# Performance work log

Hardware: AMD Instinct MI355X
Metric: run time of the kernel (lower is better)

Reference implementation:

```python
import jax, jax.numpy as jnp
import numpy as np

LOSS_WEIGHT = 1.0
BIG = 1e9  # finite sentinel for masked-out pixels (avoids inf-grad NaNs)


def setup_inputs() -> dict:
    key = jax.random.key(0)
    k1, k2 = jax.random.split(key)
    B, N, H, W = 4, 6890, 64, 64
    vert2d = jax.random.uniform(k1, (B, N, 2), dtype=jnp.float32) * jnp.array([W, H], jnp.float32)
    mask = jax.random.randint(k2, (B, H, W), 0, 2, dtype=jnp.int32)
    return {"vert2d": vert2d, "mask": mask}


def reference(vert2d, mask):
    B, N, _ = vert2d.shape
    _, H, W = mask.shape
    scale = jnp.array([W, H], vert2d.dtype)
    v = vert2d / scale  # [B,N,2], normalized
    # all pixel coords as (x, y), normalized -- the dense equivalent of torch.where points
    ys, xs = jnp.meshgrid(jnp.arange(H), jnp.arange(W), indexing="ij")
    pts = (jnp.stack([xs.ravel(), ys.ravel()], axis=-1).astype(v.dtype) / scale)  # [HW,2]
    valid = (mask.reshape(B, -1) > 0)  # [B,HW] boolean membership of each pixel
    # pairwise L2 distances: [B,N,HW]
    diff = v[:, :, None, :] - pts[None, None, :, :]
    d = jnp.sqrt(jnp.sum(diff * diff, axis=-1))
    dm = jnp.where(valid[:, None, :], d, BIG)
    # sum over mask points of min over verts  +  sum over verts of min over mask points
    loss = jnp.sum(jnp.min(dm, axis=1) * valid) + jnp.sum(jnp.min(dm, axis=2))
    return LOSS_WEIGHT * loss
```

## Files before the change

### kernel.cpp

```cpp
#include <hip/hip_runtime.h>

#define NB 4
#define NV 6890
#define HW 4096
#define NPAD 6912
#define T1CS 108
#define T1_BLOCKS 512
#define T2_BLOCKS 512
#define NELEM 44032
#define NRED_BLOCKS 16

#define OFF_T1  0
#define OFF_T2  65536

#define FINF 3.402823466e38f
#define VBIG 1.0e9f
#define PBIG 1.0e18f

__global__ __launch_bounds__(256) void k_main(const float* __restrict__ vert,
                                              const int* __restrict__ mask,
                                              unsigned* __restrict__ t1,
                                              unsigned* __restrict__ t2) {
    __shared__ float4 lds4[64];
    float2* lds2 = reinterpret_cast<float2*>(lds4);
    int bx = blockIdx.x, tid = threadIdx.x;
    if (bx < T1_BLOCKS) {
        int c = bx & 63, q = (bx >> 6) & 1, b = bx >> 7;
        if (tid < T1CS) {
            int n = c * T1CS + tid;
            float2 w = make_float2(VBIG, 0.f);
            if (n < NV) w = reinterpret_cast<const float2*>(vert)[b * NV + n];
            lds2[tid] = w;
        }
        __syncthreads();
        int x = tid & 63, ry = tid >> 6;
        float fx = (float)x;
        float fm2x = -2.f * fx, fx2 = fx * fx;
        float fm2y[8], m[8];
        #pragma unroll
        for (int k = 0; k < 8; ++k) {
            fm2y[k] = -2.f * (float)(q * 32 + ry + 4 * k);
            m[k] = FINF;
        }
        #pragma unroll 6
        for (int i = 0; i < T1CS / 2; ++i) {
            float4 a = lds4[i];
            float vva = fmaf(a.x, a.x, a.y * a.y);
            float vvb = fmaf(a.z, a.z, a.w * a.w);
            float ta  = fmaf(fm2x, a.x, vva);
            float tb  = fmaf(fm2x, a.z, vvb);
            #pragma unroll
            for (int k = 0; k < 8; ++k) {
                float da = fmaf(fm2y[k], a.y, ta);
                float db = fmaf(fm2y[k], a.w, tb);
                m[k] = fminf(m[k], fminf(da, db));
            }
        }
        unsigned* tp = t1 + (b << 12) + x;
        #pragma unroll
        for (int k = 0; k < 8; ++k) {
            int y = q * 32 + ry + 4 * k;
            float fy = (float)y;
            float mf = fmaxf(fmaf(fy, fy, fx2) + m[k], 0.f);
            atomicMin(tp + y * 64, __float_as_uint(mf));
        }
    } else {
        int t2i = bx - T1_BLOCKS;
        int y = t2i & 63, rest = t2i >> 6;
        int g = rest & 1, b = rest >> 1;
        if (tid < 64) {
            int pix = y * 64 + tid;
            float fx = (float)tid;
            float e = (mask[b * HW + pix] > 0) ? fx * fx : PBIG;
            lds2[tid] = make_float2(-2.f * fx, e);
        }
        __syncthreads();
        int n0 = g * 4096 + tid;
        const float2* vv2 = reinterpret_cast<const float2*>(vert) + b * NV;
        float fy = (float)y, fm2y = -2.f * fy;
        float vx[16], base[16], mr[16];
        bool val[16];
        #pragma unroll
        for (int k = 0; k < 16; ++k) {
            int n = n0 + 256 * k;
            val[k] = (n < NV);
            float2 t = val[k] ? vv2[n] : make_float2(0.f, 0.f);
            vx[k] = t.x;
            float vv = fmaf(t.x, t.x, t.y * t.y);
            base[k] = fmaf(fm2y, t.y, fmaf(fy, fy, vv));
            mr[k] = FINF;
        }
        #pragma unroll 4
        for (int j = 0; j < 32; ++j) {
            float4 a = lds4[j];
            #pragma unroll
            for (int k = 0; k < 16; ++k) {
                float da = fmaf(a.x, vx[k], a.y);
                float db = fmaf(a.z, vx[k], a.w);
                mr[k] = fminf(mr[k], fminf(da, db));
            }
        }
        unsigned* op = t2 + b * NPAD + n0;
        #pragma unroll
        for (int k = 0; k < 16; ++k)
            if (val[k]) {
                float mf = fmaxf(mr[k] + base[k], 0.f);
                atomicMin(op + 256 * k, __float_as_uint(mf));
            }
    }
}

__global__ __launch_bounds__(256) void k_red(const unsigned* __restrict__ t1,
                                             const unsigned* __restrict__ t2,
                                             const int* __restrict__ mask,
                                             float* __restrict__ out) {
    int tid = threadIdx.x;
    float v = 0.f;
    for (int gid = blockIdx.x * 256 + tid; gid < NELEM; gid += NRED_BLOCKS * 256) {
        float e = 0.f;
        if (gid < NB * HW) {
            if (mask[gid] > 0)
                e = sqrtf(fmaxf(__uint_as_float(t1[gid]), 0.f));
        } else {
            int j = gid - NB * HW;
            int b = j / NPAD;
            int n = j - b * NPAD;
            if (n < NV)
                e = sqrtf(fmaxf(__uint_as_float(t2[j]), 0.f));
        }
        v += e;
    }
    v *= (1.0f / 64.0f);
    __shared__ float sbuf[4];
    for (int off = 32; off; off >>= 1) v += __shfl_down(v, off, 64);
    int lane = tid & 63, wid = tid >> 6;
    if (!lane) sbuf[wid] = v;
    __syncthreads();
    if (tid == 0)
        atomicAdd(out, sbuf[0] + sbuf[1] + sbuf[2] + sbuf[3]);
}

extern "C" void kernel_launch(void* const* d_in, const int* in_sizes, int n_in,
                              void* d_out, int out_size, void* d_ws, size_t ws_size,
                              hipStream_t stream) {
    const float* vert = (const float*)d_in[0];
    const int*   mask = (const int*)d_in[1];
    char* ws = (char*)d_ws;
    unsigned* t1  = (unsigned*)(ws + OFF_T1);
    unsigned* t2  = (unsigned*)(ws + OFF_T2);
    float*    out = (float*)d_out;

    k_main<<<T1_BLOCKS + T2_BLOCKS, 256, 0, stream>>>(vert, mask, t1, t2);
    k_red <<<NRED_BLOCKS, 256, 0, stream>>>(t1, t2, mask, out);
}
```

Baseline: 73.86 us.

## Fuse chamfer min and reduction into one kernel with in-block minima

```diff
diff --git a/kernel.cpp b/kernel.cpp
--- a/kernel.cpp
+++ b/kernel.cpp
@@ -3,52 +3,95 @@
 #define NB 4
 #define NV 6890
 #define HW 4096
-#define NPAD 6912
-#define T1CS 108
-#define T1_BLOCKS 512
-#define T2_BLOCKS 512
-#define NELEM 44032
-#define NRED_BLOCKS 16
-
-#define OFF_T1  0
-#define OFF_T2  65536
-
+#define NV4 3445
+#define CH4 108
+#define CH4P 111
+#define NCHUNK 32
+#define T2_BPB 54
+#define T2_BLOCKS (NB * T2_BPB)
+#define T1_BLOCKS (NB * 64)
 #define FINF 3.402823466e38f
 #define VBIG 1.0e9f
 #define PBIG 1.0e18f
+#define INV_S (1.0f / 64.0f)
 
-__global__ __launch_bounds__(256) void k_main(const float* __restrict__ vert,
-                                              const int* __restrict__ mask,
-                                              unsigned* __restrict__ t1,
-                                              unsigned* __restrict__ t2) {
-    __shared__ float4 lds4[64];
-    float2* lds2 = reinterpret_cast<float2*>(lds4);
+__global__ __launch_bounds__(256) void k_fused(const float* __restrict__ vert,
+                                               const int* __restrict__ mask,
+                                               float* __restrict__ out) {
+    __shared__ __align__(16) char smem[65024];
     int bx = blockIdx.x, tid = threadIdx.x;
-    if (bx < T1_BLOCKS) {
-        int c = bx & 63, q = (bx >> 6) & 1, b = bx >> 7;
-        if (tid < T1CS) {
-            int n = c * T1CS + tid;
-            float2 w = make_float2(VBIG, 0.f);
-            if (n < NV) w = reinterpret_cast<const float2*>(vert)[b * NV + n];
-            lds2[tid] = w;
+    if (bx < T2_BLOCKS) {
+        float2* pt = reinterpret_cast<float2*>(smem);
+        float*  pr = reinterpret_cast<float*>(smem + 32768);
+        float*  sb = reinterpret_cast<float*>(smem + 34816);
+        int b = bx / T2_BPB, blk = bx - b * T2_BPB;
+        for (int i = tid; i < HW; i += 256) {
+            int x = i & 63;
+            float fx = (float)x;
+            float e = (mask[b * HW + i] > 0) ? fx * fx : PBIG;
+            pt[i] = make_float2(-2.f * fx, e);
+        }
+        int g = tid & 63, rq = tid >> 6;
+        int n0 = blk * 128 + 2 * g;
+        float4 vp = make_float4(0.f, 0.f, 0.f, 0.f);
+        if (n0 < NV)
+            vp = reinterpret_cast<const float4*>(vert)[(b * NV + n0) >> 1];
+        __syncthreads();
+        float vx0 = vp.x, vy0 = vp.y, vx1 = vp.z, vy1 = vp.w;
+        float vx20 = vx0 * vx0, vx21 = vx1 * vx1;
+        float m0 = FINF, m1 = FINF;
+        float fy = (float)(rq * 16);
+        for (int y = rq * 16; y < rq * 16 + 16; ++y, fy += 1.f) {
+            const float4* row = reinterpret_cast<const float4*>(pt + y * 64);
+            float r0 = FINF, r1 = FINF;
+            #pragma unroll 8
+            for (int j = 0; j < 32; ++j) {
+                float4 a = row[j];
+                r0 = fminf(r0, fminf(fmaf(a.x, vx0, a.y), fmaf(a.z, vx0, a.w)));
+                r1 = fminf(r1, fminf(fmaf(a.x, vx1, a.y), fmaf(a.z, vx1, a.w)));
+            }
+            float t0 = vy0 - fy, t1 = vy1 - fy;
+            m0 = fminf(m0, r0 + fmaf(t0, t0, vx20));
+            m1 = fminf(m1, r1 + fmaf(t1, t1, vx21));
+        }
+        reinterpret_cast<float2*>(pr)[rq * 64 + g] = make_float2(m0, m1);
+        __syncthreads();
+        float s = 0.f;
+        if (tid < 128) {
+            float mm = fminf(fminf(pr[tid], pr[128 + tid]),
+                             fminf(pr[256 + tid], pr[384 + tid]));
+            if (blk * 128 + tid < NV) s = sqrtf(fmaxf(mm, 0.f));
+        }
+        #pragma unroll
+        for (int off = 32; off; off >>= 1) s += __shfl_down(s, off, 64);
+        if ((tid & 63) == 0) sb[tid >> 6] = s;
+        __syncthreads();
+        if (tid == 0) atomicAdd(out, (sb[0] + sb[1] + sb[2] + sb[3]) * INV_S);
+    } else {
+        float4* v4 = reinterpret_cast<float4*>(smem);
+        float*  pr = reinterpret_cast<float*>(smem + 56832);
+        int t1i = bx - T2_BLOCKS;
+        int x = t1i & 63, b = t1i >> 6;
+        const float4* g4 = reinterpret_cast<const float4*>(vert) + b * NV4;
+        for (int i = tid; i < NCHUNK * CH4; i += 256) {
+            int c = i / CH4;
+            float4 w = (i < NV4) ? g4[i] : make_float4(VBIG, 0.f, VBIG, 0.f);
+            v4[i + 3 * c] = w;
         }
         __syncthreads();
-        int x = tid & 63, ry = tid >> 6;
-        float fx = (float)x;
-        float fm2x = -2.f * fx, fx2 = fx * fx;
+        int chunk = tid >> 3, ry = tid & 7;
+        float fx = (float)x, fm2x = -2.f * fx, fx2 = fx * fx;
         float fm2y[8], m[8];
         #pragma unroll
-        for (int k = 0; k < 8; ++k) {
-            fm2y[k] = -2.f * (float)(q * 32 + ry + 4 * k);
-            m[k] = FINF;
-        }
-        #pragma unroll 6
-        for (int i = 0; i < T1CS / 2; ++i) {
-            float4 a = lds4[i];
+        for (int k = 0; k < 8; ++k) { fm2y[k] = -2.f * (float)(ry + 8 * k); m[k] = FINF; }
+        const float4* cp = v4 + chunk * CH4P;
+        #pragma unroll 4
+        for (int i = 0; i < CH4; ++i) {
+            float4 a = cp[i];
             float vva = fmaf(a.x, a.x, a.y * a.y);
             float vvb = fmaf(a.z, a.z, a.w * a.w);
-            float ta  = fmaf(fm2x, a.x, vva);
-            float tb  = fmaf(fm2x, a.z, vvb);
+            float ta = fmaf(fm2x, a.x, vva);
+            float tb = fmaf(fm2x, a.z, vvb);
             #pragma unroll
             for (int k = 0; k < 8; ++k) {
                 float da = fmaf(fm2y[k], a.y, ta);
@@ -56,88 +99,23 @@
                 m[k] = fminf(m[k], fminf(da, db));
             }
         }
-        unsigned* tp = t1 + (b << 12) + x;
         #pragma unroll
-        for (int k = 0; k < 8; ++k) {
-            int y = q * 32 + ry + 4 * k;
-            float fy = (float)y;
-            float mf = fmaxf(fmaf(fy, fy, fx2) + m[k], 0.f);
-            atomicMin(tp + y * 64, __float_as_uint(mf));
-        }
-    } else {
-        int t2i = bx - T1_BLOCKS;
-        int y = t2i & 63, rest = t2i >> 6;
-        int g = rest & 1, b = rest >> 1;
+        for (int k = 0; k < 8; ++k) pr[chunk * 64 + ry + 8 * k] = m[k];
+        __syncthreads();
+        float e = 0.f;
         if (tid < 64) {
-            int pix = y * 64 + tid;
-            float fx = (float)tid;
-            float e = (mask[b * HW + pix] > 0) ? fx * fx : PBIG;
-            lds2[tid] = make_float2(-2.f * fx, e);
-        }
-        __syncthreads();
-        int n0 = g * 4096 + tid;
-        const float2* vv2 = reinterpret_cast<const float2*>(vert) + b * NV;
-        float fy = (float)y, fm2y = -2.f * fy;
-        float vx[16], base[16], mr[16];
-        bool val[16];
-        #pragma unroll
-        for (int k = 0; k < 16; ++k) {
-            int n = n0 + 256 * k;
-            val[k] = (n < NV);
-            float2 t = val[k] ? vv2[n] : make_float2(0.f, 0.f);
-            vx[k] = t.x;
-            float vv = fmaf(t.x, t.x, t.y * t.y);
-            base[k] = fmaf(fm2y, t.y, fmaf(fy, fy, vv));
-            mr[k] = FINF;
-        }
-        #pragma unroll 4
-        for (int j = 0; j < 32; ++j) {
-            float4 a = lds4[j];
+            float mv = pr[tid];
             #pragma unroll
-            for (int k = 0; k < 16; ++k) {
-                float da = fmaf(a.x, vx[k], a.y);
-                float db = fmaf(a.z, vx[k], a.w);
-                mr[k] = fminf(mr[k], fminf(da, db));
+            for (int c = 1; c < NCHUNK; ++c) mv = fminf(mv, pr[c * 64 + tid]);
+            if (mask[(b * 64 + tid) * 64 + x] > 0) {
+                float fyv = (float)tid;
+                e = sqrtf(fmaxf(mv + fmaf(fyv, fyv, fx2), 0.f));
             }
         }
-        unsigned* op = t2 + b * NPAD + n0;
         #pragma unroll
-        for (int k = 0; k < 16; ++k)
-            if (val[k]) {
-                float mf = fmaxf(mr[k] + base[k], 0.f);
-                atomicMin(op + 256 * k, __float_as_uint(mf));
-            }
+        for (int off = 32; off; off >>= 1) e += __shfl_down(e, off, 64);
+        if (tid == 0) atomicAdd(out, e * INV_S);
     }
-}
-
-__global__ __launch_bounds__(256) void k_red(const unsigned* __restrict__ t1,
-                                             const unsigned* __restrict__ t2,
-                                             const int* __restrict__ mask,
-                                             float* __restrict__ out) {
-    int tid = threadIdx.x;
-    float v = 0.f;
-    for (int gid = blockIdx.x * 256 + tid; gid < NELEM; gid += NRED_BLOCKS * 256) {
-        float e = 0.f;
-        if (gid < NB * HW) {
-            if (mask[gid] > 0)
-                e = sqrtf(fmaxf(__uint_as_float(t1[gid]), 0.f));
-        } else {
-            int j = gid - NB * HW;
-            int b = j / NPAD;
-            int n = j - b * NPAD;
-            if (n < NV)
-                e = sqrtf(fmaxf(__uint_as_float(t2[j]), 0.f));
-        }
-        v += e;
-    }
-    v *= (1.0f / 64.0f);
-    __shared__ float sbuf[4];
-    for (int off = 32; off; off >>= 1) v += __shfl_down(v, off, 64);
-    int lane = tid & 63, wid = tid >> 6;
-    if (!lane) sbuf[wid] = v;
-    __syncthreads();
-    if (tid == 0)
-        atomicAdd(out, sbuf[0] + sbuf[1] + sbuf[2] + sbuf[3]);
 }
 
 extern "C" void kernel_launch(void* const* d_in, const int* in_sizes, int n_in,
@@ -145,11 +123,6 @@
                               hipStream_t stream) {
     const float* vert = (const float*)d_in[0];
     const int*   mask = (const int*)d_in[1];
-    char* ws = (char*)d_ws;
-    unsigned* t1  = (unsigned*)(ws + OFF_T1);
-    unsigned* t2  = (unsigned*)(ws + OFF_T2);
-    float*    out = (float*)d_out;
-
-    k_main<<<T1_BLOCKS + T2_BLOCKS, 256, 0, stream>>>(vert, mask, t1, t2);
-    k_red <<<NRED_BLOCKS, 256, 0, stream>>>(t1, t2, mask, out);
+    (void)d_ws; (void)ws_size;
+    k_fused<<<T2_BLOCKS + T1_BLOCKS, 256, 0, stream>>>(vert, mask, (float*)d_out);
 }
```

Measured after the change: 71.34 us. 3.4% less time.
